# Kernel tuning notes

Measured on AMD Instinct MI355X. Metric: run time of the kernel, lower is better.

Reference implementation:

```python
import jax, jax.numpy as jnp
import numpy as np

N, D, E, TOP_K = 4096, 1024, 8, 2
NEG_INF = -1e38


def setup_inputs() -> dict:
    key = jax.random.key(0)
    ks = jax.random.split(key, 6)
    s = 1.0 / np.sqrt(D)
    return {
        "x": jax.random.normal(ks[0], (N, D), jnp.float32),
        "noise": jax.random.normal(ks[1], (E,), jnp.float32),
        "Wg": jax.random.normal(ks[2], (D, E), jnp.float32) * s,
        "Wn": jax.random.normal(ks[3], (D, E), jnp.float32) * s,
        "We": jax.random.normal(ks[4], (E, D, D), jnp.float32) * s,
        "be": jax.random.normal(ks[5], (E, D), jnp.float32) * 0.01,
    }


def reference(x, noise, Wg, Wn, We, be):
    # Gating: H = Wg(x) + randn(E) * softplus(Wnoise(x))   (Eq. 4-5)
    g = x @ Wg                                      # [N, E]
    H = g + noise[None, :] * jax.nn.softplus(x @ Wn)  # [N, E]
    # Keep top_k entries of H, set the rest to -Inf (scatter of bottom E-k)
    vals, idx = jax.lax.top_k(H, TOP_K)             # [N, k]
    keep = jnp.full_like(H, NEG_INF)
    keep = keep.at[jnp.arange(H.shape[0])[:, None], idx].set(vals)
    G = jax.nn.softmax(keep, axis=1)                # [N, E]; masked entries -> 0
    # Expert outputs; masked experts have G==0 so dense weighted sum matches
    # the sparse per-example loop: out_n = sum_j G[n,j] * expert_j(x_n)
    Y = jnp.einsum('nd,edh->neh', x, We) + be[None, :, :]  # [N, E, D]
    out = jnp.einsum('ne,neh->nh', G, Y)            # [N, D]
    return out
```

## Files before the change

### kernel.cpp

```cpp
#include <hip/hip_runtime.h>
#include <hip/hip_bf16.h>
#include <stdint.h>

#define NR   4096
#define DIM  1024
#define NE   8
#define BM   128
#define BN   128
#define BK   32

typedef __attribute__((ext_vector_type(8))) short  bf16x8;
typedef __attribute__((ext_vector_type(8))) ushort u16x8;
typedef __attribute__((ext_vector_type(4))) float  f32x4;

__device__ __forceinline__ ushort f2bf(float f) {
    union { __hip_bfloat16 h; ushort u; } cv;
    cv.h = __float2bfloat16(f);
    return cv.u;
}

__device__ __forceinline__ void gload16(const void* g, void* l) {
    __builtin_amdgcn_global_load_lds(
        (const __attribute__((address_space(1))) unsigned int*)g,
        (__attribute__((address_space(3))) unsigned int*)l, 16, 0, 0);
}

__global__ __launch_bounds__(256)
void k1_prep(const float* __restrict__ Wg, const float* __restrict__ Wn,
             float* __restrict__ WT, float* __restrict__ out) {
    const int tid = threadIdx.x;
    if (blockIdx.x < 8) {
        const int k    = blockIdx.x * 128 + (tid >> 1);
        const int half = tid & 1;
        const float* src = half ? Wn : Wg;
        const float4* s4 = (const float4*)(src + (size_t)k * NE);
        float4 a = s4[0], b = s4[1];
        float* d = WT + (size_t)half * 8 * DIM;
        d[(size_t)0 * DIM + k] = a.x; d[(size_t)1 * DIM + k] = a.y;
        d[(size_t)2 * DIM + k] = a.z; d[(size_t)3 * DIM + k] = a.w;
        d[(size_t)4 * DIM + k] = b.x; d[(size_t)5 * DIM + k] = b.y;
        d[(size_t)6 * DIM + k] = b.z; d[(size_t)7 * DIM + k] = b.w;
    } else {
        const int vb = blockIdx.x - 8;
        float4 z = {0.f, 0.f, 0.f, 0.f};
        for (int i = vb * 256 + tid; i < NR * DIM / 4; i += 512 * 256)
            ((float4*)out)[i] = z;
    }
}

__global__ __launch_bounds__(256)
void k2_main(const float* __restrict__ We, ushort* __restrict__ WeT,
             const float* __restrict__ x, const float* __restrict__ noise,
             const float* __restrict__ WT, ushort* __restrict__ xbf,
             uint32_t* __restrict__ eid, float2* __restrict__ wpair) {
    __shared__ float smem[64 * 68];
    const int tid = threadIdx.x;
    if (blockIdx.x < 2048) {
        const int b  = blockIdx.x;
        const int e  = b >> 8, kt = (b >> 4) & 15, ct = b & 15;
        const float* src = We + ((size_t)e * DIM + (size_t)kt * 64) * DIM + ct * 64;
#pragma unroll
        for (int j = 0; j < 4; ++j) {
            int idx = tid + j * 256;
            int r = idx >> 4, c4 = idx & 15;
            *(float4*)&smem[r * 68 + c4 * 4] = *(const float4*)(src + (size_t)r * DIM + c4 * 4);
        }
        __syncthreads();
        ushort* dst = WeT + ((size_t)e * DIM + (size_t)ct * 64) * DIM + kt * 64;
#pragma unroll
        for (int j = 0; j < 2; ++j) {
            int u = tid + j * 256;
            int c = u >> 3, ch = u & 7;
            ushort tmp[8];
#pragma unroll
            for (int q = 0; q < 8; ++q) tmp[q] = f2bf(smem[(ch * 8 + q) * 68 + c]);
            *(u16x8*)(dst + (size_t)c * DIM + ch * 8) = *(u16x8*)tmp;
        }
    } else {
        const int w = tid >> 6, l = tid & 63;
        const int row = (blockIdx.x - 2048) * 4 + w;
        const float* xr = x + (size_t)row * DIM;

        float4 xv[4];
#pragma unroll
        for (int q = 0; q < 4; ++q) xv[q] = *(const float4*)(xr + q * 256 + l * 4);
#pragma unroll
        for (int q = 0; q < 4; ++q) {
            ushort4 xb;
            xb.x = f2bf(xv[q].x); xb.y = f2bf(xv[q].y);
            xb.z = f2bf(xv[q].z); xb.w = f2bf(xv[q].w);
            *(ushort4*)(xbf + (size_t)row * DIM + q * 256 + l * 4) = xb;
        }

        float acc[16];
#pragma unroll
        for (int u = 0; u < 16; ++u) {
            const float* wr_ = WT + (size_t)u * DIM + l * 4;
            float s = 0.f;
#pragma unroll
            for (int q = 0; q < 4; ++q) {
                float4 wv = *(const float4*)(wr_ + q * 256);
                s += xv[q].x * wv.x + xv[q].y * wv.y + xv[q].z * wv.z + xv[q].w * wv.w;
            }
            acc[u] = s;
        }
#pragma unroll
        for (int u = 0; u < 16; ++u) smem[(w * 64 + l) * 17 + u] = acc[u];
        asm volatile("s_waitcnt lgkmcnt(0)" ::: "memory");
        const int c = l >> 4, u = l & 15;
        float v = 0.f;
#pragma unroll
        for (int i = 0; i < 16; ++i) v += smem[(w * 64 + c * 16 + i) * 17 + u];
        v += __shfl_xor(v, 16, 64);
        v += __shfl_xor(v, 32, 64);

        const int e = l & 7;
        float ag = __shfl(v, e, 64);
        float an = __shfl(v, e + 8, 64);
        float sp = (an > 0.f) ? (an + log1pf(expf(-an))) : log1pf(expf(an));
        float H  = ag + noise[e] * sp;

        float Hh[8];
#pragma unroll
        for (int k = 0; k < 8; ++k) Hh[k] = __shfl(H, k, 64);
        if (l == 0) {
            int e0 = 0; float v0 = Hh[0];
#pragma unroll
            for (int k = 1; k < 8; ++k) if (Hh[k] > v0) { v0 = Hh[k]; e0 = k; }
            int e1 = -1; float v1 = 0.f;
#pragma unroll
            for (int k = 0; k < 8; ++k)
                if (k != e0 && (e1 < 0 || Hh[k] > v1)) { v1 = Hh[k]; e1 = k; }
            float rr = expf(v1 - v0);
            float w0 = 1.f / (1.f + rr), w1 = 1.f - w0;
            eid[row] = (uint32_t)e0 | ((uint32_t)e1 << 8);
            float2 wp; wp.x = w0; wp.y = w1;
            wpair[row] = wp;
        }
    }
}

__global__ __launch_bounds__(1024)
void bucket_build(const uint32_t* __restrict__ eid, const float2* __restrict__ wpair,
                  int* __restrict__ cnt, int* __restrict__ idxl, float* __restrict__ wl) {
    const int bucket = blockIdx.x;
    const int slot = bucket >> 3, ex = bucket & 7;
    __shared__ int base;
    __shared__ int wsum[16];
    if (threadIdx.x == 0) base = 0;
    const int wid = threadIdx.x >> 6, lane = threadIdx.x & 63;
    int* bidx = idxl + (size_t)bucket * NR;
    float* bwl = wl + (size_t)bucket * NR;

    for (int c0 = 0; c0 < NR; c0 += 1024) {
        const int row = c0 + threadIdx.x;
        const uint32_t em = eid[row];
        const int e = slot ? (int)((em >> 8) & 255u) : (int)(em & 255u);
        const bool m = (e == ex);
        const unsigned long long bal = __ballot(m);
        if (lane == 0) wsum[wid] = __popcll(bal);
        __syncthreads();
        int wbase = base;
        for (int i = 0; i < wid; ++i) wbase += wsum[i];
        const int pos = wbase + __popcll(bal & ((1ull << lane) - 1ull));
        if (m) {
            bidx[pos] = row;
            float2 wp = wpair[row];
            bwl[pos]  = slot ? wp.y : wp.x;
        }
        __syncthreads();
        if (threadIdx.x == 0) {
            int s = 0;
#pragma unroll
            for (int i = 0; i < 16; ++i) s += wsum[i];
            base += s;
        }
        __syncthreads();
    }
    if (threadIdx.x == 0) cnt[bucket] = base;
}

__global__ __launch_bounds__(256, 3)
void moe_gemm(const ushort* __restrict__ xbf, const ushort* __restrict__ WeT,
              const float* __restrict__ be, const int* __restrict__ cnt,
              const int* __restrict__ idxl, const float* __restrict__ wl,
              float* __restrict__ out) {
    __shared__ ushort lds[3][256][BK];

    const int q8 = gridDim.x >> 3;
    const int W  = (blockIdx.x & 7) * q8 + (blockIdx.x >> 3);
    const int item = W >> 3, cT = W & 7;

    int bucket = -1, tile = 0, accp = 0;
#pragma unroll
    for (int b = 0; b < 16; ++b) {
        int t = (cnt[b] + BM - 1) >> 7;
        if (bucket < 0 && item < accp + t) { bucket = b; tile = item - accp; }
        accp += t;
    }
    if (bucket < 0) return;
    const int count  = cnt[bucket];
    const int nrowsv = min(BM, count - tile * BM);
    const int e  = bucket & 7;
    const int c0 = cT * BN;
    const int*   rows = idxl + (size_t)bucket * NR + tile * BM;
    const float* wrow = wl   + (size_t)bucket * NR + tile * BM;

    const int tid = threadIdx.x, wid = tid >> 6, lane = tid & 63;
    const int l16 = lane & 15, lhi = lane >> 4;
    const int wr = (wid >> 1) * 64, wc = (wid & 1) * 64;

    const int lr   = lane >> 2;
    const int fs   = ((lane >> 2) ^ (lane >> 4)) & 3;
    const int csrc = ((lane & 3) ^ fs) * 8;
    const ushort* aptr[2];
    const ushort* bptr[2];
#pragma unroll
    for (int p = 0; p < 2; ++p) {
        int ridx = p * 64 + wid * 16 + lr;
        int gr   = rows[min(ridx, nrowsv - 1)];
        aptr[p]  = xbf + (size_t)gr * DIM + csrc;
        int col  = c0 + p * 64 + wid * 16 + lr;
        bptr[p]  = WeT + ((size_t)(e * DIM + col)) * DIM + csrc;
    }

    f32x4 acc[4][4];
#pragma unroll
    for (int m = 0; m < 4; ++m)
#pragma unroll
        for (int n = 0; n < 4; ++n) { f32x4 z = {0.f, 0.f, 0.f, 0.f}; acc[m][n] = z; }

#define STAGE(T, BUF) do {                                                   \
    const int _k0 = (T) * BK;                                                \
    ushort* _b = &lds[(BUF)][0][0];                                          \
    _Pragma("unroll")                                                        \
    for (int p = 0; p < 2; ++p) {                                            \
        gload16(aptr[p] + _k0, _b + (p * 64 + wid * 16) * BK);               \
        gload16(bptr[p] + _k0, _b + (128 + p * 64 + wid * 16) * BK);         \
    }                                                                        \
} while (0)

    const int fr    = (l16 ^ (l16 >> 2)) & 3;
    const int rslot = (lhi ^ fr) * 8;

    const int NS = DIM / BK;
    STAGE(0, 0);
    STAGE(1, 1);
    int c = 0, s = 2;
    for (int t = 0; t < NS; ++t) {
        if (t + 2 < NS) {
            STAGE(t + 2, s);
            asm volatile("s_waitcnt vmcnt(8)" ::: "memory");
        } else if (t + 1 < NS) {
            asm volatile("s_waitcnt vmcnt(4)" ::: "memory");
        } else {
            asm volatile("s_waitcnt vmcnt(0)" ::: "memory");
        }
        __builtin_amdgcn_s_barrier();

        const ushort* base = &lds[c][0][0];
        bf16x8 af[4], bfr[4];
#pragma unroll
        for (int m = 0; m < 4; ++m)
            af[m] = *(const bf16x8*)(base + (wr + m * 16 + l16) * BK + rslot);
#pragma unroll
        for (int n = 0; n < 4; ++n)
            bfr[n] = *(const bf16x8*)(base + (128 + wc + n * 16 + l16) * BK + rslot);
        __builtin_amdgcn_s_setprio(1);
#pragma unroll
        for (int m = 0; m < 4; ++m)
#pragma unroll
            for (int n = 0; n < 4; ++n)
                acc[m][n] = __builtin_amdgcn_mfma_f32_16x16x32_bf16(af[m], bfr[n], acc[m][n], 0, 0, 0);
        __builtin_amdgcn_s_setprio(0);

        asm volatile("s_waitcnt lgkmcnt(0)" ::: "memory");
        __builtin_amdgcn_s_barrier();
        s = c; c = (c == 2) ? 0 : c + 1;
    }
#undef STAGE

    float bev[4];
#pragma unroll
    for (int n = 0; n < 4; ++n) bev[n] = be[(size_t)e * DIM + c0 + wc + n * 16 + l16];
#pragma unroll
    for (int m = 0; m < 4; ++m) {
#pragma unroll
        for (int r = 0; r < 4; ++r) {
            int rl = wr + m * 16 + lhi * 4 + r;
            if (rl < nrowsv) {
                int   gr = rows[rl];
                float w  = wrow[rl];
                float* op = out + (size_t)gr * DIM + c0 + wc;
#pragma unroll
                for (int n = 0; n < 4; ++n)
                    atomicAdd(&op[n * 16 + l16], w * (acc[m][n][r] + bev[n]));
            }
        }
    }
}

extern "C" void kernel_launch(void* const* d_in, const int* in_sizes, int n_in,
                              void* d_out, int out_size, void* d_ws, size_t ws_size,
                              hipStream_t stream) {
    const float* x     = (const float*)d_in[0];
    const float* noise = (const float*)d_in[1];
    const float* Wg    = (const float*)d_in[2];
    const float* Wn    = (const float*)d_in[3];
    const float* We    = (const float*)d_in[4];
    const float* be    = (const float*)d_in[5];
    float* out = (float*)d_out;

    char* w = (char*)d_ws;
    size_t off = 256;
    int*      cnt   = (int*)w;
    int*      idxl  = (int*)(w + off);      off += (size_t)2 * NE * NR * 4;
    float*    wl    = (float*)(w + off);    off += (size_t)2 * NE * NR * 4;
    uint32_t* eid   = (uint32_t*)(w + off); off += (size_t)NR * 4;
    float2*   wpair = (float2*)(w + off);   off += (size_t)NR * 8;
    off = (off + 255) & ~(size_t)255;
    float*  WT  = (float*)(w + off);  off += (size_t)16 * DIM * 4;
    ushort* xbf = (ushort*)(w + off); off += (size_t)NR * DIM * 2;
    ushort* WeT = (ushort*)(w + off); off += (size_t)NE * DIM * DIM * 2;

    k1_prep<<<520, 256, 0, stream>>>(Wg, Wn, WT, out);
    k2_main<<<3072, 256, 0, stream>>>(We, WeT, x, noise, WT, xbf, eid, wpair);
    bucket_build<<<16, 1024, 0, stream>>>(eid, wpair, cnt, idxl, wl);
    moe_gemm<<<80 * 8, 256, 0, stream>>>(xbf, WeT, be, cnt, idxl, wl, out);
}
```

Baseline: 85.38 us.

## Merge top-2 slot buckets per expert and deepen GEMM pipeline to four stages

Bucket building now groups rows by expert over both top-k slots, so each expert's GEMM tiles hold up to twice as many rows. This cuts the count of partially filled tiles and the grid shrinks from 80 to 72 items. The GEMM main loop moves to a 4-buffer LDS ring with a 3-tile prefetch distance. Each iteration is split into two half-phases that interleave A and B global-to-LDS loads with the MFMA groups. The larger LDS footprint lowers the occupancy hint from 3 to 2 blocks per CU.

```diff
diff --git a/kernel.cpp b/kernel.cpp
--- a/kernel.cpp
+++ b/kernel.cpp
@@ -143,20 +143,20 @@
 __global__ __launch_bounds__(1024)
 void bucket_build(const uint32_t* __restrict__ eid, const float2* __restrict__ wpair,
                   int* __restrict__ cnt, int* __restrict__ idxl, float* __restrict__ wl) {
-    const int bucket = blockIdx.x;
-    const int slot = bucket >> 3, ex = bucket & 7;
+    const int ex = blockIdx.x;
     __shared__ int base;
     __shared__ int wsum[16];
     if (threadIdx.x == 0) base = 0;
     const int wid = threadIdx.x >> 6, lane = threadIdx.x & 63;
-    int* bidx = idxl + (size_t)bucket * NR;
-    float* bwl = wl + (size_t)bucket * NR;
+    int* bidx = idxl + (size_t)ex * NR;
+    float* bwl = wl + (size_t)ex * NR;
 
     for (int c0 = 0; c0 < NR; c0 += 1024) {
         const int row = c0 + threadIdx.x;
         const uint32_t em = eid[row];
-        const int e = slot ? (int)((em >> 8) & 255u) : (int)(em & 255u);
-        const bool m = (e == ex);
+        const bool m0 = (int)(em & 255u) == ex;
+        const bool m1 = (int)((em >> 8) & 255u) == ex;
+        const bool m = m0 || m1;
         const unsigned long long bal = __ballot(m);
         if (lane == 0) wsum[wid] = __popcll(bal);
         __syncthreads();
@@ -166,7 +166,7 @@
         if (m) {
             bidx[pos] = row;
             float2 wp = wpair[row];
-            bwl[pos]  = slot ? wp.y : wp.x;
+            bwl[pos]  = m0 ? wp.x : wp.y;
         }
         __syncthreads();
         if (threadIdx.x == 0) {
@@ -177,15 +177,15 @@
         }
         __syncthreads();
     }
-    if (threadIdx.x == 0) cnt[bucket] = base;
-}
-
-__global__ __launch_bounds__(256, 3)
+    if (threadIdx.x == 0) cnt[ex] = base;
+}
+
+__global__ __launch_bounds__(256, 2)
 void moe_gemm(const ushort* __restrict__ xbf, const ushort* __restrict__ WeT,
               const float* __restrict__ be, const int* __restrict__ cnt,
               const int* __restrict__ idxl, const float* __restrict__ wl,
               float* __restrict__ out) {
-    __shared__ ushort lds[3][256][BK];
+    __shared__ ushort lds[4][256][BK];
 
     const int q8 = gridDim.x >> 3;
     const int W  = (blockIdx.x & 7) * q8 + (blockIdx.x >> 3);
@@ -193,7 +193,7 @@
 
     int bucket = -1, tile = 0, accp = 0;
 #pragma unroll
-    for (int b = 0; b < 16; ++b) {
+    for (int b = 0; b < NE; ++b) {
         int t = (cnt[b] + BM - 1) >> 7;
         if (bucket < 0 && item < accp + t) { bucket = b; tile = item - accp; }
         accp += t;
@@ -201,7 +201,7 @@
     if (bucket < 0) return;
     const int count  = cnt[bucket];
     const int nrowsv = min(BM, count - tile * BM);
-    const int e  = bucket & 7;
+    const int e  = bucket;
     const int c0 = cT * BN;
     const int*   rows = idxl + (size_t)bucket * NR + tile * BM;
     const float* wrow = wl   + (size_t)bucket * NR + tile * BM;
@@ -210,18 +210,16 @@
     const int l16 = lane & 15, lhi = lane >> 4;
     const int wr = (wid >> 1) * 64, wc = (wid & 1) * 64;
 
-    const int lr   = lane >> 2;
     const int fs   = ((lane >> 2) ^ (lane >> 4)) & 3;
     const int csrc = ((lane & 3) ^ fs) * 8;
     const ushort* aptr[2];
     const ushort* bptr[2];
 #pragma unroll
-    for (int p = 0; p < 2; ++p) {
-        int ridx = p * 64 + wid * 16 + lr;
-        int gr   = rows[min(ridx, nrowsv - 1)];
-        aptr[p]  = xbf + (size_t)gr * DIM + csrc;
-        int col  = c0 + p * 64 + wid * 16 + lr;
-        bptr[p]  = WeT + ((size_t)(e * DIM + col)) * DIM + csrc;
+    for (int g = 0; g < 2; ++g) {
+        int r = g * 64 + wid * 16 + (lane >> 2);
+        aptr[g] = xbf + (size_t)rows[min(r, nrowsv - 1)] * DIM + csrc;
+        int c = c0 + g * 64 + wid * 16 + (lane >> 2);
+        bptr[g] = WeT + ((size_t)(e * DIM + c)) * DIM + csrc;
     }
 
     f32x4 acc[4][4];
@@ -230,55 +228,70 @@
 #pragma unroll
         for (int n = 0; n < 4; ++n) { f32x4 z = {0.f, 0.f, 0.f, 0.f}; acc[m][n] = z; }
 
-#define STAGE(T, BUF) do {                                                   \
-    const int _k0 = (T) * BK;                                                \
-    ushort* _b = &lds[(BUF)][0][0];                                          \
-    _Pragma("unroll")                                                        \
-    for (int p = 0; p < 2; ++p) {                                            \
-        gload16(aptr[p] + _k0, _b + (p * 64 + wid * 16) * BK);               \
-        gload16(bptr[p] + _k0, _b + (128 + p * 64 + wid * 16) * BK);         \
-    }                                                                        \
+#define STAGE_A(T, BUFI) do {                                         \
+    const int _k = (T) * BK;                                          \
+    _Pragma("unroll")                                                 \
+    for (int g = 0; g < 2; ++g)                                       \
+        gload16(aptr[g] + _k, &lds[(BUFI)][g * 64 + wid * 16][0]);    \
+} while (0)
+#define STAGE_B(T, BUFI) do {                                         \
+    const int _k = (T) * BK;                                          \
+    _Pragma("unroll")                                                 \
+    for (int g = 0; g < 2; ++g)                                       \
+        gload16(bptr[g] + _k, &lds[(BUFI)][128 + g * 64 + wid * 16][0]); \
 } while (0)
 
     const int fr    = (l16 ^ (l16 >> 2)) & 3;
     const int rslot = (lhi ^ fr) * 8;
 
-    const int NS = DIM / BK;
-    STAGE(0, 0);
-    STAGE(1, 1);
-    int c = 0, s = 2;
-    for (int t = 0; t < NS; ++t) {
-        if (t + 2 < NS) {
-            STAGE(t + 2, s);
-            asm volatile("s_waitcnt vmcnt(8)" ::: "memory");
-        } else if (t + 1 < NS) {
-            asm volatile("s_waitcnt vmcnt(4)" ::: "memory");
-        } else {
-            asm volatile("s_waitcnt vmcnt(0)" ::: "memory");
-        }
+    const int NT = DIM / BK;
+    STAGE_A(0, 0); STAGE_B(0, 0);
+    STAGE_A(1, 1); STAGE_B(1, 1);
+    STAGE_A(2, 2); STAGE_B(2, 2);
+    asm volatile("s_waitcnt vmcnt(8)" ::: "memory");
+    __builtin_amdgcn_s_barrier();
+
+    for (int t = 0; t < NT; ++t) {
+        const int c = t & 3;
+        const ushort* base = &lds[c][0][0];
+        bf16x8 af0 = *(const bf16x8*)(base + (wr + 0 * 16 + l16) * BK + rslot);
+        bf16x8 af1 = *(const bf16x8*)(base + (wr + 1 * 16 + l16) * BK + rslot);
+        bf16x8 bfr[4];
+#pragma unroll
+        for (int n = 0; n < 4; ++n)
+            bfr[n] = *(const bf16x8*)(base + (128 + wc + n * 16 + l16) * BK + rslot);
+        if (t + 3 < NT) STAGE_A(t + 3, (t + 3) & 3);
         __builtin_amdgcn_s_barrier();
-
-        const ushort* base = &lds[c][0][0];
-        bf16x8 af[4], bfr[4];
-#pragma unroll
-        for (int m = 0; m < 4; ++m)
-            af[m] = *(const bf16x8*)(base + (wr + m * 16 + l16) * BK + rslot);
-#pragma unroll
-        for (int n = 0; n < 4; ++n)
-            bfr[n] = *(const bf16x8*)(base + (128 + wc + n * 16 + l16) * BK + rslot);
+        asm volatile("s_waitcnt lgkmcnt(0)" ::: "memory");
         __builtin_amdgcn_s_setprio(1);
 #pragma unroll
-        for (int m = 0; m < 4; ++m)
-#pragma unroll
-            for (int n = 0; n < 4; ++n)
-                acc[m][n] = __builtin_amdgcn_mfma_f32_16x16x32_bf16(af[m], bfr[n], acc[m][n], 0, 0, 0);
+        for (int n = 0; n < 4; ++n)
+            acc[0][n] = __builtin_amdgcn_mfma_f32_16x16x32_bf16(af0, bfr[n], acc[0][n], 0, 0, 0);
+#pragma unroll
+        for (int n = 0; n < 4; ++n)
+            acc[1][n] = __builtin_amdgcn_mfma_f32_16x16x32_bf16(af1, bfr[n], acc[1][n], 0, 0, 0);
         __builtin_amdgcn_s_setprio(0);
-
+        __builtin_amdgcn_s_barrier();
+        bf16x8 af2 = *(const bf16x8*)(base + (wr + 2 * 16 + l16) * BK + rslot);
+        bf16x8 af3 = *(const bf16x8*)(base + (wr + 3 * 16 + l16) * BK + rslot);
+        if (t + 3 < NT) STAGE_B(t + 3, (t + 3) & 3);
+        __builtin_amdgcn_s_barrier();
         asm volatile("s_waitcnt lgkmcnt(0)" ::: "memory");
+        __builtin_amdgcn_s_setprio(1);
+#pragma unroll
+        for (int n = 0; n < 4; ++n)
+            acc[2][n] = __builtin_amdgcn_mfma_f32_16x16x32_bf16(af2, bfr[n], acc[2][n], 0, 0, 0);
+#pragma unroll
+        for (int n = 0; n < 4; ++n)
+            acc[3][n] = __builtin_amdgcn_mfma_f32_16x16x32_bf16(af3, bfr[n], acc[3][n], 0, 0, 0);
+        __builtin_amdgcn_s_setprio(0);
+        if (t < NT - 3)       asm volatile("s_waitcnt vmcnt(8)" ::: "memory");
+        else if (t == NT - 3) asm volatile("s_waitcnt vmcnt(4)" ::: "memory");
+        else                  asm volatile("s_waitcnt vmcnt(0)" ::: "memory");
         __builtin_amdgcn_s_barrier();
-        s = c; c = (c == 2) ? 0 : c + 1;
-    }
-#undef STAGE
+    }
+#undef STAGE_A
+#undef STAGE_B
 
     float bev[4];
 #pragma unroll
@@ -325,6 +338,6 @@
 
     k1_prep<<<520, 256, 0, stream>>>(Wg, Wn, WT, out);
     k2_main<<<3072, 256, 0, stream>>>(We, WeT, x, noise, WT, xbf, eid, wpair);
-    bucket_build<<<16, 1024, 0, stream>>>(eid, wpair, cnt, idxl, wl);
-    moe_gemm<<<80 * 8, 256, 0, stream>>>(xbf, WeT, be, cnt, idxl, wl, out);
-}
+    bucket_build<<<NE, 1024, 0, stream>>>(eid, wpair, cnt, idxl, wl);
+    moe_gemm<<<72 * 8, 256, 0, stream>>>(xbf, WeT, be, cnt, idxl, wl, out);
+}
```

Measured after the change: 95.75 us. +12.1%, slower.
